# Performance work log

Hardware: AMD Instinct MI355X
Metric: run time of the kernel (lower is better)

Reference implementation:

```python
import jax, jax.numpy as jnp
import numpy as np

N = 12288
SQUARE_SIZE = 100.0
NEIGHBOURHOOD = 10.0
THRESHOLD = 1.0  # spiking threshold of the reconstructed Node LIF update


def _build_weights(key):
    # topology: [N, 2] points in a square of side SQUARE_SIZE
    topo = jax.random.uniform(key, (N, 2), dtype=jnp.float32) * SQUARE_SIZE
    # pairwise euclidean distances via the ||a||^2 + ||b||^2 - 2 a.b identity
    sq = jnp.sum(topo * topo, axis=1)                      # [N]
    d2 = sq[:, None] + sq[None, :] - 2.0 * (topo @ topo.T)  # [N, N]
    dist = jnp.sqrt(jnp.maximum(d2, 0.0))
    # distance-decayed weights, masked to the local neighbourhood, no self-loop
    mask = (dist < NEIGHBOURHOOD) & ~jnp.eye(N, dtype=bool)
    return jnp.where(mask, jnp.exp(-dist), 0.0).astype(jnp.float32)


def setup_inputs() -> dict:
    key = jax.random.key(0)
    k_x, k_w, k_f = jax.random.split(key, 3)
    x = jax.random.normal(k_x, (N,), dtype=jnp.float32)
    W = _build_weights(k_w)                                 # [N, N]
    is_firing = (jax.random.uniform(k_f, (N,)) < 0.1).astype(jnp.float32)
    v = jnp.zeros((N,), dtype=jnp.float32)                  # membrane potentials
    return {"x": x, "W": W, "is_firing": is_firing, "v": v}


def reference(x, W, is_firing, v):
    # Fused form of the per-node python loop:
    #   node_x[i] = node[i].get_weights() @ is_firing  (stale is_firing for all i)
    node_x = W @ is_firing                                  # [N] sparse-weighted matvec
    # Node.forward: integrate input, fire above threshold, reset fired neurons
    v_acc = v + node_x
    fire = v_acc > THRESHOLD
    v_new = jnp.where(fire, 0.0, v_acc)
    is_firing_new = fire.astype(jnp.float32)
    # original module returns x unchanged; expose updated state for checking
    return x, is_firing_new, v_new, node_x
```

## Files before the change

### kernel.cpp

```cpp
#include <hip/hip_runtime.h>


#define SPK_N      12288
#define SPK_NV4    (SPK_N / 4)
#define SPK_BLOCK  256
#define SPK_WAVES  4
#define SPK_GRID   768

__global__ __launch_bounds__(SPK_BLOCK, 1)
void spiking_layer_kernel(const float* __restrict__ x,
                          const float* __restrict__ W,
                          const float* __restrict__ f,
                          const float* __restrict__ v,
                          float* __restrict__ out)
{
    __shared__ float4 sf[SPK_NV4];

    const int tid = threadIdx.x;

    const float4* f4 = reinterpret_cast<const float4*>(f);
    #pragma unroll
    for (int k = 0; k < SPK_NV4 / SPK_BLOCK; ++k)
        sf[k * SPK_BLOCK + tid] = f4[k * SPK_BLOCK + tid];
    __syncthreads();

    const int wave  = tid >> 6;
    const int lane  = tid & 63;
    const int gwaves = SPK_GRID * SPK_WAVES;

    for (int row = blockIdx.x * SPK_WAVES + wave; row < SPK_N; row += gwaves) {
        const float4* wrow =
            reinterpret_cast<const float4*>(W + (size_t)row * SPK_N);

        float acc = 0.0f;
        #pragma unroll 8
        for (int k = 0; k < SPK_NV4 / 64; ++k) {
            const float4 wv = wrow[k * 64 + lane];
            const float4 fv = sf[k * 64 + lane];
            acc += wv.x * fv.x + wv.y * fv.y + wv.z * fv.z + wv.w * fv.w;
        }

        #pragma unroll
        for (int off = 32; off > 0; off >>= 1)
            acc += __shfl_down(acc, off, 64);

        if (lane == 0) {
            const float node_x = acc;
            const float v_acc  = v[row] + node_x;
            const bool  fire   = v_acc > 1.0f;
            out[row]               = x[row];
            out[SPK_N + row]       = fire ? 1.0f : 0.0f;
            out[2 * SPK_N + row]   = fire ? 0.0f : v_acc;
            out[3 * SPK_N + row]   = node_x;
        }
    }
}

extern "C" void kernel_launch(void* const* d_in, const int* in_sizes, int n_in,
                              void* d_out, int out_size, void* d_ws, size_t ws_size,
                              hipStream_t stream)
{
    const float* x = (const float*)d_in[0];
    const float* W = (const float*)d_in[1];
    const float* f = (const float*)d_in[2];
    const float* v = (const float*)d_in[3];
    float* out = (float*)d_out;

    spiking_layer_kernel<<<SPK_GRID, SPK_BLOCK, 0, stream>>>(x, W, f, v, out);
}
```

Before: 110.2 us.

## Process two rows per wave with bf16 shared firing vector and nontemporal W loads

Each wave now computes two fixed rows with no grid-stride loop, on a grid doubled to 1536 blocks. The firing vector is stored in shared memory as truncated bf16, which shrinks LDS per block and permits up to 5 blocks per CU. W is read with nontemporal loads so the 576MB stream does not pollute the cache. Truncating to bf16 is exact only because is_firing holds 0/1 values, so this relies on the input being binary.

```diff
diff --git a/kernel.cpp b/kernel.cpp
--- a/kernel.cpp
+++ b/kernel.cpp
@@ -2,57 +2,80 @@
 
 
 #define SPK_N      12288
-#define SPK_NV4    (SPK_N / 4)
 #define SPK_BLOCK  256
-#define SPK_WAVES  4
-#define SPK_GRID   768
+#define SPK_GRID   1536
 
-__global__ __launch_bounds__(SPK_BLOCK, 1)
+typedef float  fx4 __attribute__((ext_vector_type(4)));
+
+__global__ __launch_bounds__(SPK_BLOCK, 5)
 void spiking_layer_kernel(const float* __restrict__ x,
                           const float* __restrict__ W,
                           const float* __restrict__ f,
                           const float* __restrict__ v,
                           float* __restrict__ out)
 {
-    __shared__ float4 sf[SPK_NV4];
+    __shared__ ushort sf[SPK_N];
 
     const int tid = threadIdx.x;
 
-    const float4* f4 = reinterpret_cast<const float4*>(f);
+    const fx4* f4  = reinterpret_cast<const fx4*>(f);
+    ushort4*   sf4 = reinterpret_cast<ushort4*>(sf);
     #pragma unroll
-    for (int k = 0; k < SPK_NV4 / SPK_BLOCK; ++k)
-        sf[k * SPK_BLOCK + tid] = f4[k * SPK_BLOCK + tid];
+    for (int k = 0; k < SPK_N / 4 / SPK_BLOCK; ++k) {
+        const fx4 fv = f4[k * SPK_BLOCK + tid];
+        ushort4 u;
+        u.x = (ushort)(__float_as_uint(fv.x) >> 16);
+        u.y = (ushort)(__float_as_uint(fv.y) >> 16);
+        u.z = (ushort)(__float_as_uint(fv.z) >> 16);
+        u.w = (ushort)(__float_as_uint(fv.w) >> 16);
+        sf4[k * SPK_BLOCK + tid] = u;
+    }
     __syncthreads();
 
-    const int wave  = tid >> 6;
-    const int lane  = tid & 63;
-    const int gwaves = SPK_GRID * SPK_WAVES;
+    const int wave = tid >> 6;
+    const int lane = tid & 63;
 
-    for (int row = blockIdx.x * SPK_WAVES + wave; row < SPK_N; row += gwaves) {
-        const float4* wrow =
-            reinterpret_cast<const float4*>(W + (size_t)row * SPK_N);
+    const int r0 = blockIdx.x * 8 + wave * 2;
+    const int r1 = r0 + 1;
 
-        float acc = 0.0f;
-        #pragma unroll 8
-        for (int k = 0; k < SPK_NV4 / 64; ++k) {
-            const float4 wv = wrow[k * 64 + lane];
-            const float4 fv = sf[k * 64 + lane];
-            acc += wv.x * fv.x + wv.y * fv.y + wv.z * fv.z + wv.w * fv.w;
-        }
+    const fx4* w0 = reinterpret_cast<const fx4*>(W + (size_t)r0 * SPK_N);
+    const fx4* w1 = reinterpret_cast<const fx4*>(W + (size_t)r1 * SPK_N);
+    const ushort4* sfv = reinterpret_cast<const ushort4*>(sf);
 
-        #pragma unroll
-        for (int off = 32; off > 0; off >>= 1)
-            acc += __shfl_down(acc, off, 64);
+    float a0 = 0.0f, a1 = 0.0f;
+    #pragma unroll 4
+    for (int k = 0; k < SPK_N / 4 / 64; ++k) {
+        const int idx = k * 64 + lane;
+        const fx4 wv0 = __builtin_nontemporal_load(&w0[idx]);
+        const fx4 wv1 = __builtin_nontemporal_load(&w1[idx]);
+        const ushort4 u = sfv[idx];
+        const float fx = __uint_as_float((unsigned)u.x << 16);
+        const float fy = __uint_as_float((unsigned)u.y << 16);
+        const float fz = __uint_as_float((unsigned)u.z << 16);
+        const float fw = __uint_as_float((unsigned)u.w << 16);
+        a0 += wv0.x * fx + wv0.y * fy + wv0.z * fz + wv0.w * fw;
+        a1 += wv1.x * fx + wv1.y * fy + wv1.z * fz + wv1.w * fw;
+    }
 
-        if (lane == 0) {
-            const float node_x = acc;
-            const float v_acc  = v[row] + node_x;
-            const bool  fire   = v_acc > 1.0f;
-            out[row]               = x[row];
-            out[SPK_N + row]       = fire ? 1.0f : 0.0f;
-            out[2 * SPK_N + row]   = fire ? 0.0f : v_acc;
-            out[3 * SPK_N + row]   = node_x;
-        }
+    #pragma unroll
+    for (int off = 32; off > 0; off >>= 1) {
+        a0 += __shfl_down(a0, off, 64);
+        a1 += __shfl_down(a1, off, 64);
+    }
+
+    if (lane == 0) {
+        const float va0 = v[r0] + a0;
+        const float va1 = v[r1] + a1;
+        const bool  f0  = va0 > 1.0f;
+        const bool  f1  = va1 > 1.0f;
+        out[r0]              = x[r0];
+        out[r1]              = x[r1];
+        out[SPK_N + r0]      = f0 ? 1.0f : 0.0f;
+        out[SPK_N + r1]      = f1 ? 1.0f : 0.0f;
+        out[2 * SPK_N + r0]  = f0 ? 0.0f : va0;
+        out[2 * SPK_N + r1]  = f1 ? 0.0f : va1;
+        out[3 * SPK_N + r0]  = a0;
+        out[3 * SPK_N + r1]  = a1;
     }
 }
 
```

Result: faster. 95.15 us (-13.7%).
